# Performance work log

Hardware: AMD Instinct MI355X
Metric: run time of the kernel (lower is better)

Reference implementation:

```python
import jax, jax.numpy as jnp
import numpy as np

B, S, D_MODEL = 2, 2048, 2048
H, KVH, HD = 32, 8, 64
N_REP = H // KVH
EPS = 1e-6


def _rope_tables(seq_len, head_dim):
    pos = np.arange(seq_len, dtype=np.float32)
    inv_freq = 1.0 / (10000.0 ** (np.arange(0, head_dim, 2, dtype=np.float32) / head_dim))
    freqs = pos[:, None] * inv_freq[None, :]           # [S, HD/2]
    emb = np.concatenate([freqs, freqs], axis=-1)      # [S, HD]
    return jnp.asarray(np.cos(emb)), jnp.asarray(np.sin(emb))


def setup_inputs() -> dict:
    key = jax.random.key(0)
    ks = jax.random.split(key, 6)
    x = jax.random.normal(ks[0], (B, S, D_MODEL), jnp.float32)
    rope_cos, rope_sin = _rope_tables(S, HD)
    sc_in = 1.0 / np.sqrt(D_MODEL).astype(np.float32)
    sc_o = 1.0 / np.sqrt(H * HD).astype(np.float32)
    Wq = jax.random.normal(ks[1], (H * HD, D_MODEL), jnp.float32) * sc_in
    Wk = jax.random.normal(ks[2], (KVH * HD, D_MODEL), jnp.float32) * sc_in
    Wv = jax.random.normal(ks[3], (KVH * HD, D_MODEL), jnp.float32) * sc_in
    Wo = jax.random.normal(ks[4], (D_MODEL, H * HD), jnp.float32) * sc_o
    q_norm_w = jnp.ones((HD,), jnp.float32)
    k_norm_w = jnp.ones((HD,), jnp.float32)
    return dict(x=x, rope_cos=rope_cos, rope_sin=rope_sin, Wq=Wq, Wk=Wk, Wv=Wv,
                Wo=Wo, q_norm_w=q_norm_w, k_norm_w=k_norm_w)


def _rms_norm(x, w):
    return x * jax.lax.rsqrt(jnp.mean(x * x, axis=-1, keepdims=True) + EPS) * w


def _rotate_half(x):
    x1, x2 = jnp.split(x, 2, axis=-1)
    return jnp.concatenate((-x2, x1), axis=-1)


def reference(x, rope_cos, rope_sin, Wq, Wk, Wv, Wo, q_norm_w, k_norm_w):
    b, s, _ = x.shape
    q = (x @ Wq.T).reshape(b, s, H, HD)
    k = (x @ Wk.T).reshape(b, s, KVH, HD)
    v = (x @ Wv.T).reshape(b, s, KVH, HD)
    # per-head QK RMSNorm
    q = _rms_norm(q, q_norm_w)
    k = _rms_norm(k, k_norm_w)
    # RoPE: cos/sin [S, HD] -> broadcast over heads
    cos = rope_cos[:, None, :]
    sin = rope_sin[:, None, :]
    q = q * cos + _rotate_half(q) * sin
    k = k * cos + _rotate_half(k) * sin
    # GQA: repeat_interleave KV heads
    k = jnp.repeat(k, N_REP, axis=2)
    v = jnp.repeat(v, N_REP, axis=2)
    q = q.transpose(0, 2, 1, 3)  # [B,H,S,HD]
    k = k.transpose(0, 2, 1, 3)
    v = v.transpose(0, 2, 1, 3)
    scale = np.float32(1.0 / np.sqrt(HD))
    scores = jnp.einsum('bhqd,bhkd->bhqk', q, k) * scale
    causal = jnp.tril(jnp.ones((s, s), dtype=bool))
    scores = jnp.where(causal, scores, jnp.finfo(scores.dtype).min)
    attn = jax.nn.softmax(scores, axis=-1)
    out = jnp.einsum('bhqk,bhkd->bhqd', attn, v)
    out = out.transpose(0, 2, 1, 3).reshape(b, s, H * HD)
    return out @ Wo.T
```

## Files before the change

kernel.cpp:

```cpp
#include <hip/hip_runtime.h>
#include <stdint.h>

#define B_ 2
#define S_ 2048
#define DM_ 2048
#define H_ 32
#define KVH_ 8
#define HD_ 64
#define NQK_ 3072

typedef unsigned short u16;
typedef unsigned int u32;
typedef __attribute__((ext_vector_type(8))) short bf16x8;
typedef __attribute__((ext_vector_type(4))) float f32x4;

static __device__ __forceinline__ u16 f2bf(float f) {
  unsigned int u = __float_as_uint(f);
  u = (u + 0x7fffu + ((u >> 16) & 1u)) >> 16;
  return (u16)u;
}

static __device__ __forceinline__ void gload16(const void* g, void* lds_wave_base) {
  __builtin_amdgcn_global_load_lds(
      (__attribute__((address_space(1))) unsigned int*)(uintptr_t)g,
      (__attribute__((address_space(3))) unsigned int*)(uintptr_t)lds_wave_base,
      16, 0, 0);
}

__global__ void cvt_all(const float* __restrict__ x, const float* __restrict__ wq,
                        const float* __restrict__ wk, const float* __restrict__ wv,
                        const float* __restrict__ wo,
                        u16* __restrict__ xb, u16* __restrict__ wbq,
                        u16* __restrict__ wbo) {
  const int NX = 2097152, NQ = 1048576, NKV = 262144;
  const int TOT = NX + NQ + 2 * NKV + NQ;
  const int stride = gridDim.x * 256;
  for (int i = blockIdx.x * 256 + threadIdx.x; i < TOT; i += stride) {
    const float4* s; ushort4* d; int off;
    if (i < NX)                { s = (const float4*)x;  d = (ushort4*)xb;  off = i; }
    else if (i < NX + NQ)      { s = (const float4*)wq; d = (ushort4*)wbq; off = i - NX; }
    else if (i < NX + NQ + NKV){ s = (const float4*)wk; d = (ushort4*)(wbq + (size_t)DM_ * DM_); off = i - NX - NQ; }
    else if (i < NX + NQ + 2 * NKV) { s = (const float4*)wv; d = (ushort4*)(wbq + (size_t)DM_ * DM_ + (size_t)512 * DM_); off = i - NX - NQ - NKV; }
    else                       { s = (const float4*)wo; d = (ushort4*)wbo; off = i - NX - NQ - 2 * NKV; }
    const float4 v = s[off];
    ushort4 o;
    o.x = f2bf(v.x); o.y = f2bf(v.y); o.z = f2bf(v.z); o.w = f2bf(v.w);
    d[off] = o;
  }
}

#define BM 128
#define BN 128
#define BK 32

#define GEMM_MAIN                                                               \
  __shared__ u16 As[2][BM * BK];                                                \
  __shared__ u16 Bs[2][BN * BK];                                                \
  const int t = threadIdx.x;                                                    \
  const int lane = t & 63;                                                      \
  const int w = t >> 6;                                                         \
  const int q = lane & 15, g = lane >> 4;                                       \
  const int wr = (w >> 1) * 64, wc = (w & 1) * 64;                              \
  const int m0 = blockIdx.y * BM;                                               \
  const int n0 = blockIdx.x * BN;                                               \
  f32x4 acc[4][4] = {};                                                         \
  const char* Ab = (const char*)A;                                              \
  const char* Bb = (const char*)Bw;                                             \
  const size_t K2 = (size_t)K * 2;                                              \
  const int P0 = t * 16;                                                        \
  const int row0 = P0 >> 6, kb0 = P0 & 63;                                      \
  const int P1 = 4096 + t * 16;                                                 \
  const int row1 = P1 >> 6, kb1 = P1 & 63;                                      \
  const int Pb0 = (w << 10), Pb1 = 4096 + (w << 10);                            \
  auto STAGE = [&](int buf, int k0) {                                           \
    gload16(Ab + (size_t)(m0 + row0) * K2 + (size_t)k0 * 2 + kb0, (char*)As[buf] + Pb0); \
    gload16(Ab + (size_t)(m0 + row1) * K2 + (size_t)k0 * 2 + kb1, (char*)As[buf] + Pb1); \
    gload16(Bb + (size_t)(n0 + row0) * K2 + (size_t)k0 * 2 + kb0, (char*)Bs[buf] + Pb0); \
    gload16(Bb + (size_t)(n0 + row1) * K2 + (size_t)k0 * 2 + kb1, (char*)Bs[buf] + Pb1); \
  };                                                                            \
  STAGE(0, 0);                                                                  \
  __syncthreads();                                                              \
  int cur = 0;                                                                  \
  for (int k0 = 0; k0 < K; k0 += BK) {                                          \
    if (k0 + BK < K) STAGE(cur ^ 1, k0 + BK);                                   \
    bf16x8 af[4], bfr[4];                                                       \
    _Pragma("unroll")                                                           \
    for (int m = 0; m < 4; m++)                                                 \
      af[m] = *(const bf16x8*)((const char*)As[cur] +                           \
               (wr + m * 16 + q) * 64 + (g << 4));                              \
    _Pragma("unroll")                                                           \
    for (int n = 0; n < 4; n++)                                                 \
      bfr[n] = *(const bf16x8*)((const char*)Bs[cur] +                          \
               (wc + n * 16 + q) * 64 + (g << 4));                              \
    _Pragma("unroll")                                                           \
    for (int m = 0; m < 4; m++)                                                 \
      _Pragma("unroll")                                                         \
      for (int n = 0; n < 4; n++)                                               \
        acc[m][n] = __builtin_amdgcn_mfma_f32_16x16x32_bf16(af[m], bfr[n], acc[m][n], 0, 0, 0); \
    __syncthreads();                                                            \
    cur ^= 1;                                                                   \
  }

__global__ __launch_bounds__(256) void gemm_bt(const u16* __restrict__ A,
                                               const u16* __restrict__ Bw,
                                               float* __restrict__ C,
                                               int M, int N, int K) {
  GEMM_MAIN
#pragma unroll
  for (int m = 0; m < 4; m++) {
    const int r0 = m0 + wr + m * 16 + g * 4;
#pragma unroll
    for (int n = 0; n < 4; n++) {
      const int c = n0 + wc + n * 16 + q;
#pragma unroll
      for (int j = 0; j < 4; j++)
        C[(size_t)(r0 + j) * N + c] = acc[m][n][j];
    }
  }
}

__global__ __launch_bounds__(256) void gemm_qkv(const u16* __restrict__ A,
                                                const u16* __restrict__ Bw,
                                                u16* __restrict__ C,
                                                const float* __restrict__ cosT,
                                                const float* __restrict__ sinT,
                                                const float* __restrict__ qwv,
                                                const float* __restrict__ kwv,
                                                float qscale,
                                                int M, int N, int K) {
  GEMM_MAIN
  const int hcol = (n0 + wc) >> 6;
  const bool isV = hcol >= 40;
  const bool isQ = hcol < 32;
  const float osc = isQ ? qscale : 1.0f;
  float wgt[4] = {1.f, 1.f, 1.f, 1.f};
  if (!isV) {
    const float* wp = isQ ? qwv : kwv;
#pragma unroll
    for (int n = 0; n < 4; n++) wgt[n] = wp[n * 16 + q];
  }
#pragma unroll
  for (int m = 0; m < 4; m++) {
#pragma unroll
    for (int j = 0; j < 4; j++) {
      const int row = m0 + wr + m * 16 + g * 4 + j;
      float v[4];
#pragma unroll
      for (int n = 0; n < 4; n++) v[n] = acc[m][n][j];
      if (!isV) {
        float ss = v[0] * v[0] + v[1] * v[1] + v[2] * v[2] + v[3] * v[3];
        ss += __shfl_xor(ss, 1, 64);
        ss += __shfl_xor(ss, 2, 64);
        ss += __shfl_xor(ss, 4, 64);
        ss += __shfl_xor(ss, 8, 64);
        const float inv = rsqrtf(ss * (1.0f / 64.0f) + 1e-6f);
        const int s = row & (S_ - 1);
        float xn[4];
#pragma unroll
        for (int n = 0; n < 4; n++) xn[n] = v[n] * inv * wgt[n];
#pragma unroll
        for (int n = 0; n < 4; n++) {
          const float rot = (n < 2) ? -xn[n + 2] : xn[n - 2];
          const int d = n * 16 + q;
          v[n] = (xn[n] * cosT[s * 64 + d] + rot * sinT[s * 64 + d]) * osc;
        }
      }
#pragma unroll
      for (int n = 0; n < 4; n++)
        C[(size_t)row * N + (n0 + wc + n * 16 + q)] = f2bf(v[n]);
    }
  }
}

__global__ void v_transpose(const u16* __restrict__ QKV, u16* __restrict__ Vt) {
  __shared__ u16 tile[64][72];
  const int s0 = blockIdx.x * 64;
  const int bk = blockIdx.y;
  const int b = bk / KVH_, kvh = bk % KVH_;
  const int t = threadIdx.x;
#pragma unroll
  for (int it = 0; it < 16; it++) {
    int idx = it * 256 + t;
    int sl = idx >> 6, d = idx & 63;
    tile[sl][d] = QKV[(size_t)(b * S_ + s0 + sl) * NQK_ + 2560 + kvh * 64 + d];
  }
  __syncthreads();
#pragma unroll
  for (int it = 0; it < 16; it++) {
    int idx = it * 256 + t;
    int d = idx >> 6, sl = idx & 63;
    Vt[(((size_t)(b * KVH_ + kvh)) * HD_ + d) * S_ + s0 + sl] = tile[sl][d];
  }
}

__global__ __launch_bounds__(256, 4) void attn_fwd(const u16* __restrict__ QKV,
                                                   const u16* __restrict__ Vt,
                                                   u16* __restrict__ Out) {
  __shared__ u16 Ksm[2][64 * 64];
  __shared__ u16 Vsm[2][64 * 64];
  __shared__ u16 Psm[4][16 * 64];

  const int t = threadIdx.x, lane = t & 63, w = t >> 6;
  const int q = lane & 15, g = lane >> 4;

  const int fid = blockIdx.y * 16 + blockIdx.x;
  const int xcd = fid & 7, slot = fid >> 3;
  const int kg = xcd * 2 + (slot >> 6);
  const int sub = slot & 63;
  const int ip = sub >> 2;
  const int b = kg >> 3, kvh = kg & 7;
  const int h = kvh * 4 + (sub & 3);

  const char* Kb = (const char*)(QKV + (size_t)b * S_ * NQK_ + 2048 + kvh * 64);
  const char* Vb = (const char*)(Vt + ((size_t)(b * KVH_ + kvh)) * HD_ * S_);

  const int SP0 = t * 16, SP1 = 4096 + t * 16;
  const int srow0 = SP0 >> 7, scb0 = (SP0 ^ ((srow0 & 7) << 4)) & 127;
  const int srow1 = SP1 >> 7, scb1 = (SP1 ^ ((srow1 & 7) << 4)) & 127;
  const int SB0 = (w << 10), SB1 = 4096 + (w << 10);
  const size_t KROW = (size_t)NQK_ * 2;

  auto STAGE = [&](int buf, int kt) {
    gload16(Kb + (size_t)(kt * 64 + srow0) * KROW + scb0, (char*)Ksm[buf] + SB0);
    gload16(Kb + (size_t)(kt * 64 + srow1) * KROW + scb1, (char*)Ksm[buf] + SB1);
    gload16(Vb + (size_t)srow0 * (S_ * 2) + (size_t)kt * 128 + scb0, (char*)Vsm[buf] + SB0);
    gload16(Vb + (size_t)srow1 * (S_ * 2) + (size_t)kt * 128 + scb1, (char*)Vsm[buf] + SB1);
  };

  const int swz = (q & 7) << 4;
  int koff[4][2], voff[4][2], pwoff[4][2], proff[2];
#pragma unroll
  for (int nt = 0; nt < 4; nt++)
#pragma unroll
    for (int hh = 0; hh < 2; hh++) {
      koff[nt][hh] = ((nt * 16 + q) * 128 + hh * 64 + g * 16) ^ swz;
      voff[nt][hh] = ((nt * 16 + q) * 128 + hh * 64 + g * 16) ^ swz;
      pwoff[nt][hh] = (q * 128 + nt * 32 + g * 8 + hh * 4) ^ swz;
    }
#pragma unroll
  for (int c = 0; c < 2; c++) proff[c] = (q * 128 + c * 64 + g * 16) ^ swz;

  bf16x8 ones;
#pragma unroll
  for (int j = 0; j < 8; j++) ones[j] = (short)0x3F80;

  auto process = [&](int qt) {
    const int q0w = qt * 64 + w * 16;
    bf16x8 aq[2];
    {
      const u16* qp = QKV + (size_t)(b * S_ + q0w + q) * NQK_ + h * 64 + g * 8;
      aq[0] = *(const bf16x8*)qp;
      aq[1] = *(const bf16x8*)(qp + 32);
    }
    f32x4 o_acc[4] = {};
    f32x4 l_acc = {};

    STAGE(0, 0);
    __syncthreads();
    int cur = 0;

    for (int kt = 0; kt <= qt; kt++) {
      if (kt < qt) STAGE(cur ^ 1, kt + 1);

      f32x4 sc[4];
      __builtin_amdgcn_s_setprio(1);
#pragma unroll
      for (int nt = 0; nt < 4; nt++) {
        f32x4 s = {};
#pragma unroll
        for (int hh = 0; hh < 2; hh++) {
          bf16x8 bk = *(const bf16x8*)((const char*)Ksm[cur] + koff[nt][hh]);
          s = __builtin_amdgcn_mfma_f32_16x16x32_bf16(bk, aq[hh], s, 0, 0, 0);
        }
        sc[nt] = s;
      }
      __builtin_amdgcn_s_setprio(0);

      if (kt == qt) {
#pragma unroll
        for (int nt = 0; nt < 4; nt++)
#pragma unroll
          for (int r = 0; r < 4; r++)
            if (nt * 16 + g * 4 + r > w * 16 + q) sc[nt][r] = -1e30f;
      }

#pragma unroll
      for (int nt = 0; nt < 4; nt++)
#pragma unroll
        for (int r = 0; r < 4; r++) sc[nt][r] = exp2f(sc[nt][r] - 12.0f);
#pragma unroll
      for (int nt = 0; nt < 4; nt++)
#pragma unroll
        for (int hh = 0; hh < 2; hh++) {
          u32 wv;
          asm("v_cvt_pk_bf16_f32 %0, %1, %2"
              : "=v"(wv) : "v"(sc[nt][2 * hh]), "v"(sc[nt][2 * hh + 1]));
          *(u32*)((char*)Psm[w] + pwoff[nt][hh]) = wv;
        }

      asm volatile("s_waitcnt lgkmcnt(0)" ::: "memory");
      __builtin_amdgcn_sched_barrier(0);

      bf16x8 pa[2];
#pragma unroll
      for (int c = 0; c < 2; c++)
        pa[c] = *(const bf16x8*)((const char*)Psm[w] + proff[c]);

      __builtin_amdgcn_s_setprio(1);
      l_acc = __builtin_amdgcn_mfma_f32_16x16x32_bf16(pa[0], ones, l_acc, 0, 0, 0);
      l_acc = __builtin_amdgcn_mfma_f32_16x16x32_bf16(pa[1], ones, l_acc, 0, 0, 0);
#pragma unroll
      for (int c = 0; c < 2; c++)
#pragma unroll
        for (int dt = 0; dt < 4; dt++) {
          bf16x8 bv = *(const bf16x8*)((const char*)Vsm[cur] + voff[dt][c]);
          o_acc[dt] = __builtin_amdgcn_mfma_f32_16x16x32_bf16(pa[c], bv, o_acc[dt], 0, 0, 0);
        }
      __builtin_amdgcn_s_setprio(0);

      __syncthreads();
      cur ^= 1;
    }

#pragma unroll
    for (int r = 0; r < 4; r++) {
      const int qg = q0w + g * 4 + r;
      const float inv = 1.0f / l_acc[r];
#pragma unroll
      for (int dt = 0; dt < 4; dt++)
        Out[(((size_t)b * S_ + qg) * H_ + h) * HD_ + dt * 16 + q] =
            f2bf(o_acc[dt][r] * inv);
    }
  };

  process(ip);
  process(31 - ip);
}

extern "C" void kernel_launch(void* const* d_in, const int* in_sizes, int n_in,
                              void* d_out, int out_size, void* d_ws, size_t ws_size,
                              hipStream_t stream) {
  const float* x  = (const float*)d_in[0];
  const float* rc = (const float*)d_in[1];
  const float* rs = (const float*)d_in[2];
  const float* Wq = (const float*)d_in[3];
  const float* Wk = (const float*)d_in[4];
  const float* Wv = (const float*)d_in[5];
  const float* Wo = (const float*)d_in[6];
  const float* qw = (const float*)d_in[7];
  const float* kw = (const float*)d_in[8];
  float* out = (float*)d_out;

  char* ws = (char*)d_ws;
  const size_t MB = (size_t)1 << 20;
  u16* xb   = (u16*)(ws + 0 * MB);
  u16* wbq  = (u16*)(ws + 16 * MB);
  u16* wbo  = (u16*)(ws + 28 * MB);
  u16* QKVb = (u16*)(ws + 36 * MB);
  u16* Vtb  = (u16*)(ws + 60 * MB);
  u16* AO   = xb;

  const int MT = B_ * S_;
  const float QSC = 0.125f * 1.44269504089f;

  cvt_all<<<dim3(2048), 256, 0, stream>>>(x, Wq, Wk, Wv, Wo, xb, wbq, wbo);

  gemm_qkv<<<dim3(NQK_ / BN, MT / BM), 256, 0, stream>>>(
      xb, wbq, QKVb, rc, rs, qw, kw, QSC, MT, NQK_, DM_);

  v_transpose<<<dim3(S_ / 64, B_ * KVH_), 256, 0, stream>>>(QKVb, Vtb);

  attn_fwd<<<dim3(16, 64), 256, 0, stream>>>(QKVb, Vtb, AO);

  gemm_bt<<<dim3(DM_ / BN, MT / BM), 256, 0, stream>>>(AO, wbo, out, MT, DM_, DM_);
}
```

Measured before the change: 206.7 us.

## Share K/V tile loads between paired low and high query tiles in attention

Instead of processing the two paired query tiles (ip and 31-ip) sequentially, each reloading K/V from global memory, the kernel now walks a single K/V stream up to the high tile and applies each staged tile to both query tiles while the low tile is still active. This roughly halves global K/V staging traffic and the number of barrier-separated iterations for the low tile. It also folds the -12 exponent offset into the MFMA accumulator initial value and reuses koff for V offsets. The cost is more live registers for two sets of accumulators, which may lower occupancy.

```diff
diff --git a/kernel.cpp b/kernel.cpp
--- a/kernel.cpp
+++ b/kernel.cpp
@@ -228,13 +228,12 @@
   };
 
   const int swz = (q & 7) << 4;
-  int koff[4][2], voff[4][2], pwoff[4][2], proff[2];
+  int koff[4][2], pwoff[4][2], proff[2];
 #pragma unroll
   for (int nt = 0; nt < 4; nt++)
 #pragma unroll
     for (int hh = 0; hh < 2; hh++) {
       koff[nt][hh] = ((nt * 16 + q) * 128 + hh * 64 + g * 16) ^ swz;
-      voff[nt][hh] = ((nt * 16 + q) * 128 + hh * 64 + g * 16) ^ swz;
       pwoff[nt][hh] = (q * 128 + nt * 32 + g * 8 + hh * 4) ^ swz;
     }
 #pragma unroll
@@ -244,87 +243,96 @@
 #pragma unroll
   for (int j = 0; j < 8; j++) ones[j] = (short)0x3F80;
 
-  auto process = [&](int qt) {
-    const int q0w = qt * 64 + w * 16;
-    bf16x8 aq[2];
-    {
-      const u16* qp = QKV + (size_t)(b * S_ + q0w + q) * NQK_ + h * 64 + g * 8;
-      aq[0] = *(const bf16x8*)qp;
-      aq[1] = *(const bf16x8*)(qp + 32);
-    }
-    f32x4 o_acc[4] = {};
-    f32x4 l_acc = {};
-
-    STAGE(0, 0);
+  const int qlo = ip, qhi = 31 - ip;
+
+  bf16x8 aqL[2], aqH[2];
+  {
+    const u16* qpL = QKV + (size_t)(b * S_ + qlo * 64 + w * 16 + q) * NQK_ + h * 64 + g * 8;
+    const u16* qpH = QKV + (size_t)(b * S_ + qhi * 64 + w * 16 + q) * NQK_ + h * 64 + g * 8;
+    aqL[0] = *(const bf16x8*)qpL;
+    aqL[1] = *(const bf16x8*)(qpL + 32);
+    aqH[0] = *(const bf16x8*)qpH;
+    aqH[1] = *(const bf16x8*)(qpH + 32);
+  }
+
+  f32x4 oL[4] = {}, oH[4] = {};
+  f32x4 lL = {}, lH = {};
+
+  int cur = 0;
+
+  auto tile_step = [&](int kt, int qt, const bf16x8* aq, f32x4* o_acc, f32x4& l_acc) {
+    f32x4 sc[4];
+    __builtin_amdgcn_s_setprio(1);
+#pragma unroll
+    for (int nt = 0; nt < 4; nt++) {
+      f32x4 s = {-12.0f, -12.0f, -12.0f, -12.0f};
+#pragma unroll
+      for (int hh = 0; hh < 2; hh++) {
+        bf16x8 bk = *(const bf16x8*)((const char*)Ksm[cur] + koff[nt][hh]);
+        s = __builtin_amdgcn_mfma_f32_16x16x32_bf16(bk, aq[hh], s, 0, 0, 0);
+      }
+      sc[nt] = s;
+    }
+    __builtin_amdgcn_s_setprio(0);
+
+    if (kt == qt) {
+#pragma unroll
+      for (int nt = 0; nt < 4; nt++)
+#pragma unroll
+        for (int r = 0; r < 4; r++)
+          if (nt * 16 + g * 4 + r > w * 16 + q) sc[nt][r] = -1e30f;
+    }
+
+#pragma unroll
+    for (int nt = 0; nt < 4; nt++)
+#pragma unroll
+      for (int r = 0; r < 4; r++) sc[nt][r] = exp2f(sc[nt][r]);
+#pragma unroll
+    for (int nt = 0; nt < 4; nt++)
+#pragma unroll
+      for (int hh = 0; hh < 2; hh++) {
+        u32 wv;
+        asm("v_cvt_pk_bf16_f32 %0, %1, %2"
+            : "=v"(wv) : "v"(sc[nt][2 * hh]), "v"(sc[nt][2 * hh + 1]));
+        *(u32*)((char*)Psm[w] + pwoff[nt][hh]) = wv;
+      }
+
+    asm volatile("s_waitcnt lgkmcnt(0)" ::: "memory");
+    __builtin_amdgcn_sched_barrier(0);
+
+    bf16x8 pa[2];
+#pragma unroll
+    for (int c = 0; c < 2; c++)
+      pa[c] = *(const bf16x8*)((const char*)Psm[w] + proff[c]);
+
+    __builtin_amdgcn_s_setprio(1);
+    l_acc = __builtin_amdgcn_mfma_f32_16x16x32_bf16(pa[0], ones, l_acc, 0, 0, 0);
+    l_acc = __builtin_amdgcn_mfma_f32_16x16x32_bf16(pa[1], ones, l_acc, 0, 0, 0);
+#pragma unroll
+    for (int c = 0; c < 2; c++)
+#pragma unroll
+      for (int dt = 0; dt < 4; dt++) {
+        bf16x8 bv = *(const bf16x8*)((const char*)Vsm[cur] + koff[dt][c]);
+        o_acc[dt] = __builtin_amdgcn_mfma_f32_16x16x32_bf16(pa[c], bv, o_acc[dt], 0, 0, 0);
+      }
+    __builtin_amdgcn_s_setprio(0);
+  };
+
+  STAGE(0, 0);
+  __syncthreads();
+
+  for (int kt = 0; kt <= qhi; kt++) {
+    if (kt < qhi) STAGE(cur ^ 1, kt + 1);
+    if (kt <= qlo) tile_step(kt, qlo, aqL, oL, lL);
+    tile_step(kt, qhi, aqH, oH, lH);
     __syncthreads();
-    int cur = 0;
-
-    for (int kt = 0; kt <= qt; kt++) {
-      if (kt < qt) STAGE(cur ^ 1, kt + 1);
-
-      f32x4 sc[4];
-      __builtin_amdgcn_s_setprio(1);
-#pragma unroll
-      for (int nt = 0; nt < 4; nt++) {
-        f32x4 s = {};
-#pragma unroll
-        for (int hh = 0; hh < 2; hh++) {
-          bf16x8 bk = *(const bf16x8*)((const char*)Ksm[cur] + koff[nt][hh]);
-          s = __builtin_amdgcn_mfma_f32_16x16x32_bf16(bk, aq[hh], s, 0, 0, 0);
-        }
-        sc[nt] = s;
-      }
-      __builtin_amdgcn_s_setprio(0);
-
-      if (kt == qt) {
-#pragma unroll
-        for (int nt = 0; nt < 4; nt++)
-#pragma unroll
-          for (int r = 0; r < 4; r++)
-            if (nt * 16 + g * 4 + r > w * 16 + q) sc[nt][r] = -1e30f;
-      }
-
-#pragma unroll
-      for (int nt = 0; nt < 4; nt++)
-#pragma unroll
-        for (int r = 0; r < 4; r++) sc[nt][r] = exp2f(sc[nt][r] - 12.0f);
-#pragma unroll
-      for (int nt = 0; nt < 4; nt++)
-#pragma unroll
-        for (int hh = 0; hh < 2; hh++) {
-          u32 wv;
-          asm("v_cvt_pk_bf16_f32 %0, %1, %2"
-              : "=v"(wv) : "v"(sc[nt][2 * hh]), "v"(sc[nt][2 * hh + 1]));
-          *(u32*)((char*)Psm[w] + pwoff[nt][hh]) = wv;
-        }
-
-      asm volatile("s_waitcnt lgkmcnt(0)" ::: "memory");
-      __builtin_amdgcn_sched_barrier(0);
-
-      bf16x8 pa[2];
-#pragma unroll
-      for (int c = 0; c < 2; c++)
-        pa[c] = *(const bf16x8*)((const char*)Psm[w] + proff[c]);
-
-      __builtin_amdgcn_s_setprio(1);
-      l_acc = __builtin_amdgcn_mfma_f32_16x16x32_bf16(pa[0], ones, l_acc, 0, 0, 0);
-      l_acc = __builtin_amdgcn_mfma_f32_16x16x32_bf16(pa[1], ones, l_acc, 0, 0, 0);
-#pragma unroll
-      for (int c = 0; c < 2; c++)
-#pragma unroll
-        for (int dt = 0; dt < 4; dt++) {
-          bf16x8 bv = *(const bf16x8*)((const char*)Vsm[cur] + voff[dt][c]);
-          o_acc[dt] = __builtin_amdgcn_mfma_f32_16x16x32_bf16(pa[c], bv, o_acc[dt], 0, 0, 0);
-        }
-      __builtin_amdgcn_s_setprio(0);
-
-      __syncthreads();
-      cur ^= 1;
-    }
-
+    cur ^= 1;
+  }
+
+  auto write_out = [&](int qt, const f32x4* o_acc, const f32x4& l_acc) {
 #pragma unroll
     for (int r = 0; r < 4; r++) {
-      const int qg = q0w + g * 4 + r;
+      const int qg = qt * 64 + w * 16 + g * 4 + r;
       const float inv = 1.0f / l_acc[r];
 #pragma unroll
       for (int dt = 0; dt < 4; dt++)
@@ -332,9 +340,8 @@
             f2bf(o_acc[dt][r] * inv);
     }
   };
-
-  process(ip);
-  process(31 - ip);
+  write_out(qlo, oL, lL);
+  write_out(qhi, oH, lH);
 }
 
 extern "C" void kernel_launch(void* const* d_in, const int* in_sizes, int n_in,
```

New measurement: 203.2 us. Within noise of the previous version (-1.7%).
